# Kernel tuning notes

Hardware: AMD Instinct MI355X
Metric: run time of the kernel (lower is better)

Reference implementation:

```python
import jax, jax.numpy as jnp
import numpy as np

B, Q, D = 4, 1024, 1024
N, DH = 16, 64  # n_head, d_head
SCALE = 1.0 / DH ** 0.5
LN_EPS = 1e-5


def setup_inputs() -> dict:
    key = jax.random.key(0)
    ks = jax.random.split(key, 10)
    return {
        "w": jax.random.normal(ks[0], (B, Q, D), jnp.float32),
        "r_emb": jax.random.normal(ks[1], (Q, N, DH), jnp.float32),
        "r_w_bias": jax.random.normal(ks[2], (N, DH), jnp.float32),
        "r_bias": jax.random.normal(ks[3], (Q, N), jnp.float32),
        # projection weights stored [in, out]; torch Linear init std = 1/sqrt(d_head)
        "Wq": jax.random.normal(ks[4], (D, N * DH), jnp.float32) * SCALE,
        "Wk": jax.random.normal(ks[5], (D, N * DH), jnp.float32) * SCALE,
        "Wv": jax.random.normal(ks[6], (D, N * DH), jnp.float32) * SCALE,
        "Wo": jax.random.normal(ks[7], (N * DH, D), jnp.float32) * SCALE,
        "ln_gamma": jnp.ones((D,), jnp.float32),
        "ln_beta": jnp.zeros((D,), jnp.float32),
    }


def _rel_shift(x):
    # x: [b, i, j, n]; pad a zero column at the end of j then drop j=0
    # equivalent to shifting left by one along j with a trailing zero.
    return jnp.concatenate([x[:, :, 1:, :], jnp.zeros_like(x[:, :, :1, :])], axis=2)


def reference(w, r_emb, r_w_bias, r_bias, Wq, Wk, Wv, Wo, ln_gamma, ln_beta):
    b, qlen, d = w.shape
    klen = qlen  # mems=None
    n, dh = r_w_bias.shape

    q_h = (w @ Wq).reshape(b, qlen, n, dh)
    k_h = (w @ Wk).reshape(b, klen, n, dh)
    v_h = (w @ Wv).reshape(b, klen, n, dh)

    rw_q = q_h + r_w_bias[None, None]                      # [b,q,n,dh]
    AC = jnp.einsum('bind,bjnd->bijn', rw_q, k_h)          # [b,q,k,n]
    B_ = jnp.einsum('bind,jnd->bijn', q_h, r_emb)          # [b,q,k,n]
    BD = _rel_shift(B_ + r_bias[None, None])               # [b,q,k,n]

    attn_score = (AC + BD) * SCALE
    attn_prob = jax.nn.softmax(attn_score, axis=2)
    attn_vec = jnp.einsum('bijn,bjnd->bind', attn_prob, v_h)
    attn_out = attn_vec.reshape(b, qlen, n * dh) @ Wo

    out = w + attn_out  # residual (post-lnorm path)
    mu = jnp.mean(out, axis=-1, keepdims=True)
    var = jnp.var(out, axis=-1, keepdims=True)
    return (out - mu) / jnp.sqrt(var + LN_EPS) * ln_gamma + ln_beta
```

## Files before the change

kernel.cpp:

```cpp
#include <hip/hip_runtime.h>
#include <hip/hip_bf16.h>

using f16 = _Float16;
typedef _Float16 f16x8 __attribute__((ext_vector_type(8)));
typedef _Float16 f16x4 __attribute__((ext_vector_type(4)));
typedef float f32x4 __attribute__((ext_vector_type(4)));

#define AS1 __attribute__((address_space(1)))
#define AS3 __attribute__((address_space(3)))

constexpr int Bc = 4, Qc = 1024, Dc = 1024, Nh = 16, DHc = 64;
constexpr int BQ = Bc * Qc;
constexpr int NHEAD = Bc * Nh;
constexpr float ATT_SCALE = 0.125f;

__global__ void k_f2h(const float* __restrict__ src, f16* __restrict__ dst) {
    long i8 = ((long)blockIdx.x * blockDim.x + threadIdx.x) * 8;
    float4 a = *(const float4*)&src[i8];
    float4 b = *(const float4*)&src[i8 + 4];
    f16x8 o = { (f16)a.x, (f16)a.y, (f16)a.z, (f16)a.w,
                (f16)b.x, (f16)b.y, (f16)b.z, (f16)b.w };
    *(f16x8*)&dst[i8] = o;
}

struct Ptr4 { const float* p[4]; };
__global__ void k_transpose4(Ptr4 srcs, f16* __restrict__ dst) {
    __shared__ f16 tile[32][33];
    const float* src = srcs.p[blockIdx.z];
    f16* d = dst + (long)blockIdx.z * Dc * Dc;
    int c0 = blockIdx.x * 32, r0 = blockIdx.y * 32;
#pragma unroll
    for (int dy = 0; dy < 32; dy += 8) {
        int r = r0 + threadIdx.y + dy, c = c0 + threadIdx.x;
        tile[threadIdx.y + dy][threadIdx.x] = (f16)src[(long)r * Dc + c];
    }
    __syncthreads();
#pragma unroll
    for (int dy = 0; dy < 32; dy += 8) {
        int c = c0 + threadIdx.y + dy, r = r0 + threadIdx.x;
        d[(long)c * Dc + r] = tile[threadIdx.x][threadIdx.y + dy];
    }
}

__global__ void k_fill_remb(const float* __restrict__ remb, f16* __restrict__ Ke) {
    long gid = (long)blockIdx.x * blockDim.x + threadIdx.x;
    int d8 = (int)(gid & 7) * 8;
    int j = (int)((gid >> 3) & 1023);
    int h = (int)(gid >> 13);
    int n = h & 15;
    f16x8 kv;
    if (j < 1023) {
        const float* rp = &remb[((long)(j + 1) * 16 + n) * 64 + d8];
        float4 r0 = *(const float4*)rp, r1 = *(const float4*)(rp + 4);
        kv[0] = (f16)r0.x; kv[1] = (f16)r0.y; kv[2] = (f16)r0.z; kv[3] = (f16)r0.w;
        kv[4] = (f16)r1.x; kv[5] = (f16)r1.y; kv[6] = (f16)r1.z; kv[7] = (f16)r1.w;
    } else {
        kv = f16x8{};
    }
    *(f16x8*)&Ke[(((long)h << 10) + j) * 64 + d8] = kv;
}

template <int BM, int BN, int BK, int WROWS, int WCOLS, int EPI>
__global__ __launch_bounds__(256) void k_gemm_nt(
    const f16* __restrict__ A, const f16* __restrict__ Bt, void* __restrict__ Cv,
    f16* __restrict__ qtp, f16* __restrict__ ktp, f16* __restrict__ vtp,
    int lda, int ldb, int ldc, int K)
{
    constexpr int TM = BM / (WROWS * 16);
    constexpr int TN = BN / (WCOLS * 16);
    __shared__ __align__(16) f16 sA[BM * BK];
    __shared__ __align__(16) f16 sB[BN * BK];

    const int tid = threadIdx.x;
    const int lane = tid & 63, wave = tid >> 6;
    const int wm = wave / WCOLS, wn = wave % WCOLS;
    const int m0 = blockIdx.y * BM, n0 = blockIdx.x * BN;

    f32x4 acc[TM][TN] = {};

    const int lrow = lane & 15;
    const int kq = (lane >> 4) * 8;
    const int srow = lane >> 2;
    const int scol = (lane & 3) * 8;

    for (int k0 = 0; k0 < K; k0 += BK) {
        __syncthreads();
        constexpr int CHA = BM * BK / 512;
#pragma unroll
        for (int ch = 0; ch < CHA / 4; ++ch) {
            int cc = ch * 4 + wave;
            __builtin_amdgcn_global_load_lds(
                (const AS1 void*)(const void*)&A[(long)(m0 + cc * 16 + srow) * lda + k0 + scol],
                (AS3 void*)(void*)&sA[cc * 512], 16, 0, 0);
        }
        constexpr int CHB = BN * BK / 512;
#pragma unroll
        for (int ch = 0; ch < CHB / 4; ++ch) {
            int cc = ch * 4 + wave;
            __builtin_amdgcn_global_load_lds(
                (const AS1 void*)(const void*)&Bt[(long)(n0 + cc * 16 + srow) * ldb + k0 + scol],
                (AS3 void*)(void*)&sB[cc * 512], 16, 0, 0);
        }
        __syncthreads();

        f16x8 af[TM], bfr[TN];
#pragma unroll
        for (int mi = 0; mi < TM; ++mi)
            af[mi] = *(const f16x8*)&sA[(wm * TM * 16 + mi * 16 + lrow) * BK + kq];
#pragma unroll
        for (int ni = 0; ni < TN; ++ni)
            bfr[ni] = *(const f16x8*)&sB[(wn * TN * 16 + ni * 16 + lrow) * BK + kq];
#pragma unroll
        for (int mi = 0; mi < TM; ++mi)
#pragma unroll
            for (int ni = 0; ni < TN; ++ni)
                acc[mi][ni] = __builtin_amdgcn_mfma_f32_16x16x32_f16(af[mi], bfr[ni], acc[mi][ni], 0, 0, 0);
    }

    const int crow = (lane >> 4) * 4;
    const int ccol = lane & 15;
#pragma unroll
    for (int mi = 0; mi < TM; ++mi)
#pragma unroll
        for (int ni = 0; ni < TN; ++ni)
#pragma unroll
            for (int r = 0; r < 4; ++r) {
                int gm = m0 + wm * TM * 16 + mi * 16 + crow + r;
                int gn = n0 + wn * TN * 16 + ni * 16 + ccol;
                float val = acc[mi][ni][r];
                if constexpr (EPI == 0) {
                    ((f16*)Cv)[(long)gm * ldc + gn] = (f16)val;
                } else {
                    int seg = n0 >> 10;
                    int col = gn & 1023;
                    if (seg == 0) {
                        qtp[(long)gm * 1024 + col] = (f16)val;
                    } else if (seg == 1) {
                        ktp[(long)gm * 1024 + col] = (f16)val;
                    } else {
                        int b = gm >> 10, i = gm & 1023;
                        vtp[(((long)(b << 10) + col) << 10) + i] = (f16)val;
                    }
                }
            }
}

__global__ __launch_bounds__(512, 4) void k_flash(
    const f16* __restrict__ qh, const f16* __restrict__ kh,
    const f16* __restrict__ Ke, const f16* __restrict__ vT,
    const float* __restrict__ rwb, const float* __restrict__ r_bias,
    f16* __restrict__ avp)
{
    constexpr int LDL = 136;
    __shared__ __align__(16) f16 sK[128 * LDL];
    __shared__ __align__(16) f16 sV[64 * LDL];
    __shared__ float sRB[128];

    const int tid = threadIdx.x, lane = tid & 63, wave = tid >> 6;
    const int bid = blockIdx.x;
    const int h = (((bid >> 3) & 7) << 3) | (bid & 7);
    const int i0 = (bid >> 6) * 128;
    const int b = h >> 4, n = h & 15;

    const f16* Vh = vT + (long)h * DHc * Qc;

    const int lrow = lane & 15;
    const int quad = lane >> 4;

    f16x8 rw0, rw1;
#pragma unroll
    for (int e = 0; e < 8; ++e) {
        rw0[e] = (f16)(rwb[n * 64 + quad * 8 + e] * ATT_SCALE);
        rw1[e] = (f16)(rwb[n * 64 + 32 + quad * 8 + e] * ATT_SCALE);
    }

    const f16 qsc = (f16)0.125f;
    f16x8 aq[4];
    {
        long rix = (long)(b * Qc + i0 + wave * 16 + lrow) * 1024 + n * 64;
        f16x8 q0 = *(const f16x8*)&qh[rix + quad * 8] * qsc;
        f16x8 q1 = *(const f16x8*)&qh[rix + 32 + quad * 8] * qsc;
        aq[0] = q0 + rw0;
        aq[1] = q1 + rw1;
        aq[2] = q0;
        aq[3] = q1;
    }

    float m_i = -1e30f, l_i = 0.0f;
    f32x4 o_acc[4] = {};

    for (int j0 = 0; j0 < Qc; j0 += 128) {
        __syncthreads();
        for (int idx = tid; idx < 1024; idx += 512) {
            int r = idx >> 3, c = (idx & 7) * 8;
            *(uint4*)&sK[r * LDL + c] =
                *(const uint4*)&kh[(long)(b * Qc + j0 + r) * 1024 + n * 64 + c];
            *(uint4*)&sK[r * LDL + 64 + c] =
                *(const uint4*)&Ke[((long)h * Qc + j0 + r) * 64 + c];
        }
        for (int idx = tid; idx < 64 * 16; idx += 512) {
            int r = idx >> 4, c = (idx & 15) * 8;
            *(uint4*)&sV[r * LDL + c] = *(const uint4*)&Vh[(long)r * Qc + j0 + c];
        }
        if (tid < 128) {
            int j = j0 + tid;
            sRB[tid] = (j < Qc - 1) ? r_bias[(j + 1) * Nh + n] * ATT_SCALE : 0.0f;
        }
        __syncthreads();

        f32x4 s_acc[8] = {};
#pragma unroll
        for (int kc = 0; kc < 4; ++kc)
#pragma unroll
            for (int ni = 0; ni < 8; ++ni) {
                f16x8 bk = *(const f16x8*)&sK[(ni * 16 + lrow) * LDL + kc * 32 + quad * 8];
                s_acc[ni] = __builtin_amdgcn_mfma_f32_16x16x32_f16(bk, aq[kc], s_acc[ni], 0, 0, 0);
            }

        f16x4 pf[8];
        float mx = -1e30f;
#pragma unroll
        for (int ni = 0; ni < 8; ++ni) {
            f32x4 rb4 = *(const f32x4*)&sRB[ni * 16 + quad * 4];
#pragma unroll
            for (int r = 0; r < 4; ++r) {
                float v = s_acc[ni][r] + rb4[r];
                s_acc[ni][r] = v;
                mx = fmaxf(mx, v);
            }
        }
        mx = fmaxf(mx, __shfl_xor(mx, 16));
        mx = fmaxf(mx, __shfl_xor(mx, 32));
        float mn = fmaxf(m_i, mx);
        float alpha = __expf(m_i - mn);
        float sm = 0.0f;
#pragma unroll
        for (int ni = 0; ni < 8; ++ni) {
            float e0 = __expf(s_acc[ni][0] - mn);
            float e1 = __expf(s_acc[ni][1] - mn);
            float e2 = __expf(s_acc[ni][2] - mn);
            float e3 = __expf(s_acc[ni][3] - mn);
            sm += (e0 + e1) + (e2 + e3);
            f16x4 pvv; pvv[0] = (f16)e0; pvv[1] = (f16)e1; pvv[2] = (f16)e2; pvv[3] = (f16)e3;
            pf[ni] = pvv;
        }
        sm += __shfl_xor(sm, 16);
        sm += __shfl_xor(sm, 32);
        l_i = l_i * alpha + sm;
        m_i = mn;

#pragma unroll
        for (int r = 0; r < 4; ++r) {
            float al = __shfl(alpha, quad * 4 + r);
#pragma unroll
            for (int dt = 0; dt < 4; ++dt) o_acc[dt][r] *= al;
        }

#pragma unroll
        for (int nj = 0; nj < 8; ++nj)
#pragma unroll
            for (int dt = 0; dt < 4; ++dt) {
                f16x4 bv = *(const f16x4*)&sV[(dt * 16 + lrow) * LDL + nj * 16 + quad * 4];
                o_acc[dt] = __builtin_amdgcn_mfma_f32_16x16x16f16(pf[nj], bv, o_acc[dt], 0, 0, 0);
            }
    }

    {
        float linv = 1.0f / l_i;
#pragma unroll
        for (int r = 0; r < 4; ++r) {
            float li = __shfl(linv, quad * 4 + r);
            int i = i0 + wave * 16 + quad * 4 + r;
#pragma unroll
            for (int dt = 0; dt < 4; ++dt) {
                int d = dt * 16 + lrow;
                avp[((long)(b * Qc + i) << 10) + n * 64 + d] = (f16)(o_acc[dt][r] * li);
            }
        }
    }
}

__global__ __launch_bounds__(256) void k_res_ln(const float* __restrict__ w, const f16* __restrict__ ao,
                                                const float* __restrict__ gamma, const float* __restrict__ beta,
                                                float* __restrict__ out) {
    const long base = (long)blockIdx.x * 1024;
    const int tid = threadIdx.x;
    float4 wv = *(const float4*)&w[base + tid * 4];
    f16x4 av = *(const f16x4*)&ao[base + tid * 4];
    float x[4] = { wv.x + (float)av[0], wv.y + (float)av[1],
                   wv.z + (float)av[2], wv.w + (float)av[3] };
    float s = x[0] + x[1] + x[2] + x[3];
    float s2 = x[0] * x[0] + x[1] * x[1] + x[2] * x[2] + x[3] * x[3];
#pragma unroll
    for (int off = 32; off; off >>= 1) { s += __shfl_down(s, off); s2 += __shfl_down(s2, off); }
    __shared__ float rs[4], rs2[4];
    if ((tid & 63) == 0) { rs[tid >> 6] = s; rs2[tid >> 6] = s2; }
    __syncthreads();
    s = rs[0] + rs[1] + rs[2] + rs[3];
    s2 = rs2[0] + rs2[1] + rs2[2] + rs2[3];
    float mu = s * (1.0f / 1024.0f);
    float var = s2 * (1.0f / 1024.0f) - mu * mu;
    float inv = rsqrtf(var + 1e-5f);
    float4 gv = *(const float4*)&gamma[tid * 4];
    float4 bv = *(const float4*)&beta[tid * 4];
    float4 o;
    o.x = (x[0] - mu) * inv * gv.x + bv.x;
    o.y = (x[1] - mu) * inv * gv.y + bv.y;
    o.z = (x[2] - mu) * inv * gv.z + bv.z;
    o.w = (x[3] - mu) * inv * gv.w + bv.w;
    *(float4*)&out[base + tid * 4] = o;
}

extern "C" void kernel_launch(void* const* d_in, const int* in_sizes, int n_in,
                              void* d_out, int out_size, void* d_ws, size_t ws_size,
                              hipStream_t stream) {
    const float* w_in   = (const float*)d_in[0];
    const float* r_emb  = (const float*)d_in[1];
    const float* r_wb   = (const float*)d_in[2];
    const float* r_bias = (const float*)d_in[3];
    const float* Wq     = (const float*)d_in[4];
    const float* Wk     = (const float*)d_in[5];
    const float* Wv     = (const float*)d_in[6];
    const float* Wo     = (const float*)d_in[7];
    const float* ln_g   = (const float*)d_in[8];
    const float* ln_b   = (const float*)d_in[9];
    float* out = (float*)d_out;

    char* p = (char*)d_ws;
    auto alloc = [&](size_t bytes) { char* r = p; p += (bytes + 255) & ~(size_t)255; return r; };
    f16* wh = (f16*)alloc((size_t)BQ * Dc * 2);
    f16* WT = (f16*)alloc((size_t)4 * Dc * Dc * 2);
    f16* qh = (f16*)alloc((size_t)BQ * Dc * 2);
    f16* kh = (f16*)alloc((size_t)BQ * Dc * 2);
    f16* Ke = (f16*)alloc((size_t)NHEAD * Qc * DHc * 2);
    f16* vT = (f16*)alloc((size_t)BQ * Dc * 2);
    f16* WoT = WT + (size_t)3 * Dc * Dc;
    f16* avp = wh;
    f16* ao  = Ke;

    k_f2h<<<(BQ * Dc) / (256 * 8), 256, 0, stream>>>(w_in, wh);

    Ptr4 srcs{{Wq, Wk, Wv, Wo}};
    k_transpose4<<<dim3(32, 32, 4), dim3(32, 8), 0, stream>>>(srcs, WT);

    k_fill_remb<<<(NHEAD * Qc * 8) / 256, 256, 0, stream>>>(r_emb, Ke);

    k_gemm_nt<128, 128, 32, 2, 2, 5><<<dim3(3 * Dc / 128, BQ / 128), 256, 0, stream>>>(
        wh, WT, nullptr, qh, kh, vT, Dc, Dc, 0, Dc);

    k_flash<<<512, 512, 0, stream>>>(qh, kh, Ke, vT, r_wb, r_bias, avp);

    k_gemm_nt<64, 128, 32, 2, 2, 0><<<dim3(Dc / 128, BQ / 64), 256, 0, stream>>>(
        avp, WoT, ao, nullptr, nullptr, nullptr, Dc, Dc, Dc, Dc);

    k_res_ln<<<BQ, 256, 0, stream>>>(w_in, ao, ln_g, ln_b, out);
}
```

Before: 218.6 us.

## Double-buffer flash K/V tiles with async global-to-LDS loads and XOR swizzle

The flash attention loop now processes 64-key tiles instead of 128-key tiles. K, rel-emb and V^T tiles are prefetched into double-buffered LDS with `global_load_lds` DMA while the current tile is computed. A fixed XOR swizzle replaces the padded LDS rows to avoid bank conflicts, and one barrier per tile replaces two. The aim is to hide global load latency behind the MFMA and softmax work. The risks are that the smaller tiles double the number of softmax-rescale steps and barriers, and that correctness depends on the async LDS writes being complete at the barrier.

After: 216.6 us. No clear change (-0.9%).

```diff
diff --git a/kernel.cpp b/kernel.cpp
--- a/kernel.cpp
+++ b/kernel.cpp
@@ -151,10 +151,10 @@
     const float* __restrict__ rwb, const float* __restrict__ r_bias,
     f16* __restrict__ avp)
 {
-    constexpr int LDL = 136;
-    __shared__ __align__(16) f16 sK[128 * LDL];
-    __shared__ __align__(16) f16 sV[64 * LDL];
-    __shared__ float sRB[128];
+    __shared__ __align__(16) f16 sKa[2][64 * 64];
+    __shared__ __align__(16) f16 sKe[2][64 * 64];
+    __shared__ __align__(16) f16 sVa[2][64 * 64];
+    __shared__ float sRB[2][64];
 
     const int tid = threadIdx.x, lane = tid & 63, wave = tid >> 6;
     const int bid = blockIdx.x;
@@ -162,10 +162,14 @@
     const int i0 = (bid >> 6) * 128;
     const int b = h >> 4, n = h & 15;
 
-    const f16* Vh = vT + (long)h * DHc * Qc;
-
     const int lrow = lane & 15;
     const int quad = lane >> 4;
+    const int lr3 = lane >> 3;
+    const int swc = (lane & 7) ^ (lr3 & 7);
+
+    const f16* srcK = kh + ((long)(b * Qc) + 8 * wave + lr3) * 1024 + n * 64 + swc * 8;
+    const f16* srcE = Ke + ((long)h * Qc + 8 * wave + lr3) * 64 + swc * 8;
+    const f16* srcV = vT + (long)h * DHc * Qc + (long)(8 * wave + lr3) * Qc + swc * 8;
 
     f16x8 rw0, rw1;
 #pragma unroll
@@ -189,39 +193,58 @@
     float m_i = -1e30f, l_i = 0.0f;
     f32x4 o_acc[4] = {};
 
-    for (int j0 = 0; j0 < Qc; j0 += 128) {
-        __syncthreads();
-        for (int idx = tid; idx < 1024; idx += 512) {
-            int r = idx >> 3, c = (idx & 7) * 8;
-            *(uint4*)&sK[r * LDL + c] =
-                *(const uint4*)&kh[(long)(b * Qc + j0 + r) * 1024 + n * 64 + c];
-            *(uint4*)&sK[r * LDL + 64 + c] =
-                *(const uint4*)&Ke[((long)h * Qc + j0 + r) * 64 + c];
-        }
-        for (int idx = tid; idx < 64 * 16; idx += 512) {
-            int r = idx >> 4, c = (idx & 15) * 8;
-            *(uint4*)&sV[r * LDL + c] = *(const uint4*)&Vh[(long)r * Qc + j0 + c];
-        }
-        if (tid < 128) {
-            int j = j0 + tid;
-            sRB[tid] = (j < Qc - 1) ? r_bias[(j + 1) * Nh + n] * ATT_SCALE : 0.0f;
-        }
-        __syncthreads();
-
-        f32x4 s_acc[8] = {};
-#pragma unroll
-        for (int kc = 0; kc < 4; ++kc)
-#pragma unroll
-            for (int ni = 0; ni < 8; ++ni) {
-                f16x8 bk = *(const f16x8*)&sK[(ni * 16 + lrow) * LDL + kc * 32 + quad * 8];
-                s_acc[ni] = __builtin_amdgcn_mfma_f32_16x16x32_f16(bk, aq[kc], s_acc[ni], 0, 0, 0);
-            }
-
-        f16x4 pf[8];
+    {
+        float rbv = 0.0f;
+        if (tid < 64) rbv = r_bias[(tid + 1) * Nh + n] * ATT_SCALE;
+        __builtin_amdgcn_global_load_lds((const AS1 void*)srcK, (AS3 void*)&sKa[0][wave * 512], 16, 0, 0);
+        __builtin_amdgcn_global_load_lds((const AS1 void*)srcE, (AS3 void*)&sKe[0][wave * 512], 16, 0, 0);
+        __builtin_amdgcn_global_load_lds((const AS1 void*)srcV, (AS3 void*)&sVa[0][wave * 512], 16, 0, 0);
+        if (tid < 64) sRB[0][tid] = rbv;
+    }
+    __syncthreads();
+
+    for (int jt = 0; jt < 16; ++jt) {
+        const int cur = jt & 1;
+
+        float rbn = 0.0f;
+        if (jt < 15) {
+            const int j0n = (jt + 1) * 64;
+            __builtin_amdgcn_global_load_lds((const AS1 void*)(srcK + (long)j0n * 1024),
+                                             (AS3 void*)&sKa[cur ^ 1][wave * 512], 16, 0, 0);
+            __builtin_amdgcn_global_load_lds((const AS1 void*)(srcE + (long)j0n * 64),
+                                             (AS3 void*)&sKe[cur ^ 1][wave * 512], 16, 0, 0);
+            __builtin_amdgcn_global_load_lds((const AS1 void*)(srcV + j0n),
+                                             (AS3 void*)&sVa[cur ^ 1][wave * 512], 16, 0, 0);
+            if (tid < 64) {
+                int j = j0n + tid;
+                rbn = (j < Qc - 1) ? r_bias[(j + 1) * Nh + n] * ATT_SCALE : 0.0f;
+            }
+        }
+
+        const f16* Ka = &sKa[cur][0];
+        const f16* Kb = &sKe[cur][0];
+        const f16* Va = &sVa[cur][0];
+        const int rsw = lrow & 7;
+
+        f32x4 s_acc[4] = {};
+#pragma unroll
+        for (int ni = 0; ni < 4; ++ni) {
+            int rb_ = (ni * 16 + lrow) * 64;
+            f16x8 a0 = *(const f16x8*)&Ka[rb_ + ((0 + quad) ^ rsw) * 8];
+            f16x8 a1 = *(const f16x8*)&Ka[rb_ + ((4 + quad) ^ rsw) * 8];
+            f16x8 e0 = *(const f16x8*)&Kb[rb_ + ((0 + quad) ^ rsw) * 8];
+            f16x8 e1 = *(const f16x8*)&Kb[rb_ + ((4 + quad) ^ rsw) * 8];
+            s_acc[ni] = __builtin_amdgcn_mfma_f32_16x16x32_f16(a0, aq[0], s_acc[ni], 0, 0, 0);
+            s_acc[ni] = __builtin_amdgcn_mfma_f32_16x16x32_f16(a1, aq[1], s_acc[ni], 0, 0, 0);
+            s_acc[ni] = __builtin_amdgcn_mfma_f32_16x16x32_f16(e0, aq[2], s_acc[ni], 0, 0, 0);
+            s_acc[ni] = __builtin_amdgcn_mfma_f32_16x16x32_f16(e1, aq[3], s_acc[ni], 0, 0, 0);
+        }
+
+        f16x4 pf[4];
         float mx = -1e30f;
 #pragma unroll
-        for (int ni = 0; ni < 8; ++ni) {
-            f32x4 rb4 = *(const f32x4*)&sRB[ni * 16 + quad * 4];
+        for (int ni = 0; ni < 4; ++ni) {
+            f32x4 rb4 = *(const f32x4*)&sRB[cur][ni * 16 + quad * 4];
 #pragma unroll
             for (int r = 0; r < 4; ++r) {
                 float v = s_acc[ni][r] + rb4[r];
@@ -235,7 +258,7 @@
         float alpha = __expf(m_i - mn);
         float sm = 0.0f;
 #pragma unroll
-        for (int ni = 0; ni < 8; ++ni) {
+        for (int ni = 0; ni < 4; ++ni) {
             float e0 = __expf(s_acc[ni][0] - mn);
             float e1 = __expf(s_acc[ni][1] - mn);
             float e2 = __expf(s_acc[ni][2] - mn);
@@ -257,12 +280,19 @@
         }
 
 #pragma unroll
-        for (int nj = 0; nj < 8; ++nj)
+        for (int nj = 0; nj < 4; ++nj) {
+            int coff = ((2 * nj + (quad >> 1)) ^ rsw) * 8 + (quad & 1) * 4;
 #pragma unroll
             for (int dt = 0; dt < 4; ++dt) {
-                f16x4 bv = *(const f16x4*)&sV[(dt * 16 + lrow) * LDL + nj * 16 + quad * 4];
+                f16x4 bv = *(const f16x4*)&Va[(dt * 16 + lrow) * 64 + coff];
                 o_acc[dt] = __builtin_amdgcn_mfma_f32_16x16x16f16(pf[nj], bv, o_acc[dt], 0, 0, 0);
             }
+        }
+
+        if (jt < 15) {
+            if (tid < 64) sRB[cur ^ 1][tid] = rbn;
+            __syncthreads();
+        }
     }
 
     {
```
